# Performance work log

Hardware: AMD Instinct MI355X
Metric: run time of the kernel (lower is better)

The kernel has to match this reference:

```python
import jax, jax.numpy as jnp
import numpy as np

B, S, H = 2, 2048, 3072
NQ, NKV, HD = 24, 8, 128
ROT = 96  # floor(128 * 0.75)
BASE = 10000.0


def _rope(x, rotary_dim, base=BASE, start_index=0):
    # x: [b, s, h, rotary_dim]; keras_hub GPT-NeoX style half-rotation
    s = x.shape[1]
    inv_freq = 1.0 / (base ** (jnp.arange(0, rotary_dim, 2, dtype=jnp.float32) / rotary_dim))
    pos = jnp.arange(s, dtype=jnp.float32) + start_index
    freq = pos[:, None] * inv_freq[None, :]            # [s, rot/2]
    emb = jnp.concatenate([freq, freq], axis=-1)       # [s, rot]
    cos = jnp.cos(emb)[None, :, None, :]
    sin = jnp.sin(emb)[None, :, None, :]
    x1, x2 = jnp.split(x, 2, axis=-1)
    half_rot = jnp.concatenate([-x2, x1], axis=-1)
    return x * cos + half_rot * sin


def setup_inputs() -> dict:
    key = jax.random.key(0)
    k1, k2, k3, k4, k5 = jax.random.split(key, 5)
    hidden_states = jax.random.normal(k1, (B, S, H), dtype=jnp.float32)
    # causal mask [B, S, S]
    attention_mask = jnp.broadcast_to(jnp.tril(jnp.ones((S, S), dtype=bool)), (B, S, S))
    scale = 0.02
    Wq = jax.random.normal(k2, (H, NQ, HD), dtype=jnp.float32) * scale
    Wk = jax.random.normal(k3, (H, NKV, HD), dtype=jnp.float32) * scale
    Wv = jax.random.normal(k4, (H, NKV, HD), dtype=jnp.float32) * scale
    Wo = jax.random.normal(k5, (NQ, HD, H), dtype=jnp.float32) * scale
    return {"hidden_states": hidden_states, "attention_mask": attention_mask,
            "Wq": Wq, "Wk": Wk, "Wv": Wv, "Wo": Wo}


def reference(hidden_states, attention_mask, Wq, Wk, Wv, Wo):
    groups = NQ // NKV
    inv_norm = 1.0 / np.sqrt(HD)
    q = jnp.einsum('bqm,muh->bquh', hidden_states, Wq)   # [B,S,NQ,HD]
    k = jnp.einsum('bkm,mvh->bkvh', hidden_states, Wk)   # [B,S,NKV,HD]
    v = jnp.einsum('bkm,mvh->bkvh', hidden_states, Wv)
    # partial RoPE on first ROT dims
    q = jnp.concatenate([_rope(q[..., :ROT], ROT), q[..., ROT:]], axis=-1)
    k = jnp.concatenate([_rope(k[..., :ROT], ROT), k[..., ROT:]], axis=-1)
    # GQA: repeat kv heads (interleaved, matches ops.repeat axis=2)
    k = jnp.repeat(k, groups, axis=2)
    v = jnp.repeat(v, groups, axis=2)
    scores = jnp.einsum('bquh,bkuh->buqk', q, k) * inv_norm  # [B,NQ,S,S]
    scores = scores.astype(jnp.float32)
    scores = jnp.where(attention_mask[:, None, :, :], scores, -1e9)
    probs = jax.nn.softmax(scores, axis=-1).astype(hidden_states.dtype)
    attn = jnp.einsum('buqk,bkuh->bquh', probs, v)           # [B,S,NQ,HD]
    return jnp.einsum('bquh,uhm->bqm', attn, Wo)             # [B,S,H]
```

## Files before the change

### kernel.cpp

```cpp
#include <hip/hip_runtime.h>
#include <hip/hip_bf16.h>
#include <cstdint>

namespace {

constexpr int Bn = 2, Sn = 2048, Hn = 3072, NQn = 24, NKVn = 8, HDn = 128;
constexpr int LDQKV = NQn * HDn + 2 * NKVn * HDn;
constexpr int KCOLo = NQn * HDn;
constexpr int VCOLo = KCOLo + NKVn * HDn;

typedef __attribute__((ext_vector_type(8))) __bf16 bf16x8;
typedef __attribute__((ext_vector_type(4))) float f32x4;
typedef __attribute__((ext_vector_type(4))) unsigned short u16x4;

__device__ __forceinline__ unsigned short f2bf(float f) {
  union { float f; unsigned u; } v; v.f = f;
  return (unsigned short)((v.u + 0x7fffu + ((v.u >> 16) & 1u)) >> 16);
}
__device__ __forceinline__ float bf2f(unsigned short u) {
  union { unsigned u; float f; } v; v.u = ((unsigned)u) << 16;
  return v.f;
}
__device__ __forceinline__ void gload_lds16(const void* g, void* l) {
  __builtin_amdgcn_global_load_lds(
      (__attribute__((address_space(1))) void*)(uintptr_t)g,
      (__attribute__((address_space(3))) void*)(uintptr_t)l, 16, 0, 0);
}

__global__ void build_rope_tab(float* __restrict__ cosT, float* __restrict__ sinT) {
  int idx = blockIdx.x * 256 + threadIdx.x;
  if (idx >= Sn * 48) return;
  int s = idx / 48, i = idx % 48;
  float invf = exp2f(-(float)i * (13.287712379549449f / 48.f));
  float f = (float)s * invf;
  cosT[idx] = cosf(f);
  sinT[idx] = sinf(f);
}

__global__ void cvt_f32_bf16(const float* __restrict__ in, unsigned short* __restrict__ out, int n) {
  int i = (blockIdx.x * 256 + threadIdx.x) * 4;
  int stride = gridDim.x * 256 * 4;
  for (; i < n; i += stride) {
    float4 v = *(const float4*)&in[i];
    u16x4 o;
    o[0] = f2bf(v.x); o[1] = f2bf(v.y); o[2] = f2bf(v.z); o[3] = f2bf(v.w);
    *(u16x4*)&out[i] = o;
  }
}

__global__ void transpose_cvt(const float* __restrict__ in, unsigned short* __restrict__ out,
                              int K, int N) {
  __shared__ float tile[32][33];
  int bx = blockIdx.x * 32;
  int by = blockIdx.y * 32;
  int tx = threadIdx.x & 31, ty = threadIdx.x >> 5;
#pragma unroll
  for (int r = ty; r < 32; r += 8)
    tile[r][tx] = in[(size_t)(by + r) * N + bx + tx];
  __syncthreads();
#pragma unroll
  for (int r = ty; r < 32; r += 8)
    out[(size_t)(bx + r) * K + by + tx] = f2bf(tile[tx][r]);
}

__global__ void transpose_v(const unsigned short* __restrict__ QKV, unsigned short* __restrict__ VT) {
  __shared__ unsigned short tile[32][33];
  int s0 = blockIdx.x * 32;
  int b = blockIdx.y >> 5;
  int vc0 = (blockIdx.y & 31) * 32;
  int tx = threadIdx.x & 31, ty = threadIdx.x >> 5;
#pragma unroll
  for (int r = ty; r < 32; r += 8)
    tile[r][tx] = QKV[(size_t)(b * Sn + s0 + r) * LDQKV + VCOLo + vc0 + tx];
  __syncthreads();
#pragma unroll
  for (int r = ty; r < 32; r += 8)
    VT[(size_t)(b * (NKVn * HDn) + vc0 + r) * Sn + s0 + tx] = tile[tx][r];
}

template <int BF16OUT>
__launch_bounds__(512, 1)
__global__ void gemm256(const unsigned short* __restrict__ A, const unsigned short* __restrict__ Bm,
                        void* __restrict__ Cout, int M, int N, int K) {
  __shared__ unsigned short Al[2][256 * 64];
  __shared__ unsigned short Bl[2][256 * 64];
  const int t = threadIdx.x;
  const int lane = t & 63;
  const int w = t >> 6;
  const int wm = w >> 2, wn = w & 3;
  const int l15 = lane & 15, lq = lane >> 4;
  const int brow = blockIdx.y * 256, bcol = blockIdx.x * 256;
  const unsigned short* Ab = A + (size_t)brow * K;
  const unsigned short* Bb = Bm + (size_t)bcol * K;
  f32x4 acc[8][4] = {};
  const int nT = K >> 6;

  auto stage = [&](int kt, int buf) {
#pragma unroll
    for (int it = 0; it < 4; ++it) {
      int c = it * 512 + t;
      int row = c >> 3, pos = c & 7;
      int j = pos ^ (row & 7);
      gload_lds16(Ab + (size_t)row * K + kt * 64 + j * 8, (char*)&Al[buf][0] + c * 16);
    }
#pragma unroll
    for (int it = 0; it < 4; ++it) {
      int c = it * 512 + t;
      int row = c >> 3, pos = c & 7;
      int j = pos ^ (row & 7);
      gload_lds16(Bb + (size_t)row * K + kt * 64 + j * 8, (char*)&Bl[buf][0] + c * 16);
    }
  };

  stage(0, 0);
  stage(1, 1);
  for (int kt = 0; kt < nT; ++kt) {
    if (kt + 1 < nT) asm volatile("s_waitcnt vmcnt(8)" ::: "memory");
    else             asm volatile("s_waitcnt vmcnt(0)" ::: "memory");
    __builtin_amdgcn_s_barrier();
    __builtin_amdgcn_sched_barrier(0);
    const unsigned short* Abl = &Al[kt & 1][0];
    const unsigned short* Bbl = &Bl[kt & 1][0];
#pragma unroll
    for (int ks = 0; ks < 2; ++ks) {
      bf16x8 aF[8], bF[4];
      const int j = ks * 4 + lq;
#pragma unroll
      for (int m = 0; m < 8; ++m) {
        int row = wm * 128 + m * 16 + l15;
        aF[m] = *(const bf16x8*)&Abl[row * 64 + (j ^ (row & 7)) * 8];
      }
#pragma unroll
      for (int n = 0; n < 4; ++n) {
        int row = wn * 64 + n * 16 + l15;
        bF[n] = *(const bf16x8*)&Bbl[row * 64 + (j ^ (row & 7)) * 8];
      }
      __builtin_amdgcn_s_setprio(1);
#pragma unroll
      for (int m = 0; m < 8; ++m)
#pragma unroll
        for (int n = 0; n < 4; ++n)
          acc[m][n] = __builtin_amdgcn_mfma_f32_16x16x32_bf16(aF[m], bF[n], acc[m][n], 0, 0, 0);
      __builtin_amdgcn_s_setprio(0);
    }
    asm volatile("s_waitcnt lgkmcnt(0)" ::: "memory");
    __builtin_amdgcn_s_barrier();
    __builtin_amdgcn_sched_barrier(0);
    if (kt + 2 < nT) stage(kt + 2, kt & 1);
  }

  const int lr = lq * 4;
  if (BF16OUT) {
    unsigned short* C = (unsigned short*)Cout;
#pragma unroll
    for (int m = 0; m < 8; ++m) {
      int row = brow + wm * 128 + m * 16 + lr;
#pragma unroll
      for (int n = 0; n < 4; ++n) {
        int col = bcol + wn * 64 + n * 16 + l15;
#pragma unroll
        for (int i = 0; i < 4; ++i)
          C[(size_t)(row + i) * N + col] = f2bf(acc[m][n][i]);
      }
    }
  } else {
    float* C = (float*)Cout;
#pragma unroll
    for (int m = 0; m < 8; ++m) {
      int row = brow + wm * 128 + m * 16 + lr;
#pragma unroll
      for (int n = 0; n < 4; ++n) {
        int col = bcol + wn * 64 + n * 16 + l15;
#pragma unroll
        for (int i = 0; i < 4; ++i)
          C[(size_t)(row + i) * N + col] = acc[m][n][i];
      }
    }
  }
}

__global__ void rope_kernel(unsigned short* __restrict__ QKV, const float* __restrict__ cosT,
                            const float* __restrict__ sinT) {
  int rid = blockIdx.x;
  int s = rid & (Sn - 1);
  unsigned short* row = QKV + (size_t)rid * LDQKV;
  for (int p = threadIdx.x; p < 32 * 48; p += 256) {
    int h = p / 48, i = p % 48;
    int col = (h < NQn) ? h * HDn : KCOLo + (h - NQn) * HDn;
    float c = cosT[s * 48 + i], sn = sinT[s * 48 + i];
    float x1 = bf2f(row[col + i]), x2 = bf2f(row[col + i + 48]);
    row[col + i] = f2bf(x1 * c - x2 * sn);
    row[col + i + 48] = f2bf(x2 * c + x1 * sn);
  }
}

__launch_bounds__(256, 2)
__global__ void attn_kernel(const unsigned short* __restrict__ QKV,
                            const unsigned short* __restrict__ VT,
                            unsigned short* __restrict__ O) {
  __shared__ unsigned short Klds[2][64 * 128];
  __shared__ unsigned short Vlds[2][128 * 64];
  __shared__ unsigned short Plds[4][16 * 64];
  const int t = threadIdx.x, lane = t & 63, w = t >> 6;
  const int bq = gridDim.x - 1 - blockIdx.x;
  const int hid = blockIdx.y;
  const int b = hid / NQn, u = hid % NQn, kv = u / 3;
  const int l15 = lane & 15, lh = lane >> 4;

  bf16x8 qf[4];
  {
    int qrow = bq * 64 + w * 16 + l15;
    const unsigned short* qp = QKV + (size_t)(b * Sn + qrow) * LDQKV + u * HDn;
#pragma unroll
    for (int f = 0; f < 4; ++f) qf[f] = *(const bf16x8*)(qp + f * 32 + lh * 8);
  }
  float m_l = -1e30f, l_l = 0.f;
  f32x4 Oa[8] = {};
  const float cscale = 0.08838834764831845f * 1.4426950408889634f;

  const unsigned short* Kg = QKV + (size_t)(b * Sn) * LDQKV + KCOLo + kv * HDn;
  const unsigned short* Vg = VT + (size_t)(b * NKVn + kv) * HDn * Sn;

  auto stageK = [&](int kt, int buf) {
#pragma unroll
    for (int iter = 0; iter < 4; ++iter) {
      int c = iter * 256 + t;
      int krow = c >> 4, pch = c & 15;
      int hch = (pch & 8) | ((pch & 7) ^ (krow & 7));
      gload_lds16(Kg + (size_t)(kt * 64 + krow) * LDQKV + hch * 8,
                  (char*)&Klds[buf][0] + (iter * 256 + w * 64) * 16);
    }
  };
  auto stageV = [&](int kt, int buf) {
#pragma unroll
    for (int iter = 0; iter < 4; ++iter) {
      int c = iter * 256 + t;
      int hd = c >> 3, p = c & 7;
      int sch = p ^ (hd & 7);
      gload_lds16(Vg + (size_t)hd * Sn + kt * 64 + sch * 8,
                  (char*)&Vlds[buf][0] + (iter * 256 + w * 64) * 16);
    }
  };

  const int nt = bq + 1;
  stageK(0, 0);
  stageV(0, 0);
  __syncthreads();

  for (int kt = 0; kt < nt; ++kt) {
    const int cur = kt & 1;
    if (kt + 1 < nt) { stageK(kt + 1, cur ^ 1); stageV(kt + 1, cur ^ 1); }
    const unsigned short* Kb = &Klds[cur][0];
    const unsigned short* Vb = &Vlds[cur][0];
    f32x4 Sg[4] = {};
    __builtin_amdgcn_s_setprio(1);
#pragma unroll
    for (int g = 0; g < 4; ++g) {
      int kcol = g * 16 + l15;
#pragma unroll
      for (int s = 0; s < 4; ++s) {
        int h = s * 4 + lh;
        int p = (h & 8) | ((h & 7) ^ (kcol & 7));
        bf16x8 kf = *(const bf16x8*)&Kb[kcol * 128 + p * 8];
        Sg[g] = __builtin_amdgcn_mfma_f32_16x16x32_bf16(kf, qf[s], Sg[g], 0, 0, 0);
      }
    }
    __builtin_amdgcn_s_setprio(0);
    float P[4][4];
    const bool last = (kt == bq);
    const int qin = w * 16 + l15;
#pragma unroll
    for (int g = 0; g < 4; ++g)
#pragma unroll
      for (int i = 0; i < 4; ++i) {
        float sv = Sg[g][i] * cscale;
        if (last && (g * 16 + lh * 4 + i) > qin) sv = -1e30f;
        P[g][i] = sv;
      }
    float pmax = -1e30f;
#pragma unroll
    for (int g = 0; g < 4; ++g)
#pragma unroll
      for (int i = 0; i < 4; ++i) pmax = fmaxf(pmax, P[g][i]);
    pmax = fmaxf(pmax, __shfl_xor(pmax, 16, 64));
    pmax = fmaxf(pmax, __shfl_xor(pmax, 32, 64));
    float mn = fmaxf(m_l, pmax);
    float rs = exp2f(m_l - mn);
    m_l = mn;
    float ps = 0.f;
#pragma unroll
    for (int g = 0; g < 4; ++g)
#pragma unroll
      for (int i = 0; i < 4; ++i) {
        float e = exp2f(P[g][i] - mn);
        P[g][i] = e;
        ps += e;
      }
    ps += __shfl_xor(ps, 16, 64);
    ps += __shfl_xor(ps, 32, 64);
    l_l = l_l * rs + ps;
#pragma unroll
    for (int g = 0; g < 8; ++g)
#pragma unroll
      for (int i = 0; i < 4; ++i) Oa[g][i] *= rs;
    unsigned short* pl = Plds[w];
#pragma unroll
    for (int g = 0; g < 4; ++g) {
      int ch = g * 2 + (lh >> 1);
      int pos = ch ^ (l15 & 7);
      u16x4 pk;
#pragma unroll
      for (int i = 0; i < 4; ++i) pk[i] = f2bf(P[g][i]);
      *(u16x4*)&pl[l15 * 64 + pos * 8 + (lh & 1) * 4] = pk;
    }
    __builtin_amdgcn_s_setprio(1);
#pragma unroll
    for (int kk = 0; kk < 2; ++kk) {
      int ch = kk * 4 + lh;
      bf16x8 pf = *(const bf16x8*)&pl[l15 * 64 + ((ch ^ (l15 & 7)) & 7) * 8];
#pragma unroll
      for (int g = 0; g < 8; ++g) {
        int hd = g * 16 + l15;
        int vpos = (ch ^ (hd & 7)) & 7;
        bf16x8 vf = *(const bf16x8*)&Vb[hd * 64 + vpos * 8];
        Oa[g] = __builtin_amdgcn_mfma_f32_16x16x32_bf16(vf, pf, Oa[g], 0, 0, 0);
      }
    }
    __builtin_amdgcn_s_setprio(0);
    __syncthreads();
  }
  {
    unsigned short* sc = (unsigned short*)Klds + w * 2176;
    float inv = 1.0f / l_l;
#pragma unroll
    for (int g = 0; g < 8; ++g)
#pragma unroll
      for (int i = 0; i < 4; ++i)
        sc[l15 * 136 + g * 16 + lh * 4 + i] = f2bf(Oa[g][i] * inv);
    int q = lane >> 2, a = lane & 3;
    int row = bq * 64 + w * 16 + q;
    unsigned short* op = O + (size_t)(b * Sn + row) * (NQn * HDn) + u * HDn;
    const unsigned short* scr = sc + q * 136;
#pragma unroll
    for (int j = 0; j < 4; ++j) {
      bf16x8 v = *(const bf16x8*)&scr[a * 8 + j * 32];
      *(bf16x8*)&op[a * 8 + j * 32] = v;
    }
  }
}

}

extern "C" void kernel_launch(void* const* d_in, const int* in_sizes, int n_in,
                              void* d_out, int out_size, void* d_ws, size_t ws_size,
                              hipStream_t stream) {
  const float* hidden = (const float*)d_in[0];
  const float* Wq = (const float*)d_in[2];
  const float* Wk = (const float*)d_in[3];
  const float* Wv = (const float*)d_in[4];
  const float* Wo = (const float*)d_in[5];
  float* out = (float*)d_out;

  char* ws = (char*)d_ws;
  constexpr size_t szXb = (size_t)Bn * Sn * Hn * 2;
  constexpr size_t szWqkv = (size_t)LDQKV * Hn * 2;
  constexpr size_t szWo = (size_t)Hn * Hn * 2;
  constexpr size_t szVT = (size_t)Bn * NKVn * HDn * Sn * 2;
  constexpr size_t szQKV = (size_t)Bn * Sn * LDQKV * 2;
  constexpr size_t szTab = (size_t)Sn * 48 * 4;
  static_assert(szWo + szVT <= szWqkv, "Wob+VT must fit in Wqkv region");
  constexpr size_t szTotal = szXb + szWqkv + szQKV + 2 * szTab;
  if (ws_size < szTotal) return;

  unsigned short* Xb = (unsigned short*)(ws);
  unsigned short* Obuf = Xb;
  unsigned short* Wqkv = (unsigned short*)(ws + szXb);
  unsigned short* Wob = Wqkv;
  unsigned short* VT = (unsigned short*)(ws + szXb + szWo);
  unsigned short* QKV = (unsigned short*)(ws + szXb + szWqkv);
  float* cosT = (float*)(ws + szXb + szWqkv + szQKV);
  float* sinT = (float*)(ws + szXb + szWqkv + szQKV + szTab);

  build_rope_tab<<<(Sn * 48 + 255) / 256, 256, 0, stream>>>(cosT, sinT);
  cvt_f32_bf16<<<3072, 256, 0, stream>>>(hidden, Xb, Bn * Sn * Hn);
  transpose_cvt<<<dim3(96, 96), 256, 0, stream>>>(Wq, Wqkv, Hn, NQn * HDn);
  transpose_cvt<<<dim3(32, 96), 256, 0, stream>>>(Wk, Wqkv + (size_t)KCOLo * Hn, Hn, NKVn * HDn);
  transpose_cvt<<<dim3(32, 96), 256, 0, stream>>>(Wv, Wqkv + (size_t)VCOLo * Hn, Hn, NKVn * HDn);
  gemm256<1><<<dim3(LDQKV / 256, (Bn * Sn) / 256), 512, 0, stream>>>(Xb, Wqkv, QKV,
                                                                     Bn * Sn, LDQKV, Hn);
  transpose_cvt<<<dim3(96, 96), 256, 0, stream>>>(Wo, Wob, Hn, Hn);
  transpose_v<<<dim3(Sn / 32, Bn * NKVn * HDn / 32), 256, 0, stream>>>(QKV, VT);
  rope_kernel<<<Bn * Sn, 256, 0, stream>>>(QKV, cosT, sinT);
  attn_kernel<<<dim3(Sn / 64, Bn * NQn), 256, 0, stream>>>(QKV, VT, Obuf);
  gemm256<0><<<dim3(Hn / 256, (Bn * Sn) / 256), 512, 0, stream>>>(Obuf, Wob, out,
                                                                  Bn * Sn, Hn, Hn);
}
```

Baseline: 675.7 us.

## Double query tile per attention block to reuse K/V fragments across two subtiles

```diff
diff --git a/kernel.cpp b/kernel.cpp
--- a/kernel.cpp
+++ b/kernel.cpp
@@ -198,24 +198,27 @@
 __global__ void attn_kernel(const unsigned short* __restrict__ QKV,
                             const unsigned short* __restrict__ VT,
                             unsigned short* __restrict__ O) {
-  __shared__ unsigned short Klds[2][64 * 128];
-  __shared__ unsigned short Vlds[2][128 * 64];
-  __shared__ unsigned short Plds[4][16 * 64];
+  __shared__ __align__(16) char smem[81920];
+  unsigned short* Klds = (unsigned short*)smem;
+  unsigned short* Vlds = (unsigned short*)(smem + 32768);
+  unsigned short* Plds = (unsigned short*)(smem + 65536);
   const int t = threadIdx.x, lane = t & 63, w = t >> 6;
   const int bq = gridDim.x - 1 - blockIdx.x;
   const int hid = blockIdx.y;
   const int b = hid / NQn, u = hid % NQn, kv = u / 3;
   const int l15 = lane & 15, lh = lane >> 4;
-
-  bf16x8 qf[4];
-  {
-    int qrow = bq * 64 + w * 16 + l15;
+  const int q0 = bq * 128 + w * 32;
+
+  bf16x8 qf[2][4];
+#pragma unroll
+  for (int qs = 0; qs < 2; ++qs) {
+    int qrow = q0 + qs * 16 + l15;
     const unsigned short* qp = QKV + (size_t)(b * Sn + qrow) * LDQKV + u * HDn;
 #pragma unroll
-    for (int f = 0; f < 4; ++f) qf[f] = *(const bf16x8*)(qp + f * 32 + lh * 8);
-  }
-  float m_l = -1e30f, l_l = 0.f;
-  f32x4 Oa[8] = {};
+    for (int f = 0; f < 4; ++f) qf[qs][f] = *(const bf16x8*)(qp + f * 32 + lh * 8);
+  }
+  float m_l[2] = {-1e30f, -1e30f}, l_l[2] = {0.f, 0.f};
+  f32x4 Oa[2][8] = {};
   const float cscale = 0.08838834764831845f * 1.4426950408889634f;
 
   const unsigned short* Kg = QKV + (size_t)(b * Sn) * LDQKV + KCOLo + kv * HDn;
@@ -228,7 +231,7 @@
       int krow = c >> 4, pch = c & 15;
       int hch = (pch & 8) | ((pch & 7) ^ (krow & 7));
       gload_lds16(Kg + (size_t)(kt * 64 + krow) * LDQKV + hch * 8,
-                  (char*)&Klds[buf][0] + (iter * 256 + w * 64) * 16);
+                  (char*)Klds + buf * 16384 + (iter * 256 + w * 64) * 16);
     }
   };
   auto stageV = [&](int kt, int buf) {
@@ -238,11 +241,11 @@
       int hd = c >> 3, p = c & 7;
       int sch = p ^ (hd & 7);
       gload_lds16(Vg + (size_t)hd * Sn + kt * 64 + sch * 8,
-                  (char*)&Vlds[buf][0] + (iter * 256 + w * 64) * 16);
+                  (char*)Vlds + buf * 16384 + (iter * 256 + w * 64) * 16);
     }
   };
 
-  const int nt = bq + 1;
+  const int nt = 2 * bq + 2;
   stageK(0, 0);
   stageV(0, 0);
   __syncthreads();
@@ -250,101 +253,113 @@
   for (int kt = 0; kt < nt; ++kt) {
     const int cur = kt & 1;
     if (kt + 1 < nt) { stageK(kt + 1, cur ^ 1); stageV(kt + 1, cur ^ 1); }
-    const unsigned short* Kb = &Klds[cur][0];
-    const unsigned short* Vb = &Vlds[cur][0];
-    f32x4 Sg[4] = {};
-    __builtin_amdgcn_s_setprio(1);
-#pragma unroll
-    for (int g = 0; g < 4; ++g) {
-      int kcol = g * 16 + l15;
-#pragma unroll
-      for (int s = 0; s < 4; ++s) {
-        int h = s * 4 + lh;
-        int p = (h & 8) | ((h & 7) ^ (kcol & 7));
-        bf16x8 kf = *(const bf16x8*)&Kb[kcol * 128 + p * 8];
-        Sg[g] = __builtin_amdgcn_mfma_f32_16x16x32_bf16(kf, qf[s], Sg[g], 0, 0, 0);
-      }
-    }
-    __builtin_amdgcn_s_setprio(0);
-    float P[4][4];
-    const bool last = (kt == bq);
-    const int qin = w * 16 + l15;
-#pragma unroll
-    for (int g = 0; g < 4; ++g)
-#pragma unroll
-      for (int i = 0; i < 4; ++i) {
-        float sv = Sg[g][i] * cscale;
-        if (last && (g * 16 + lh * 4 + i) > qin) sv = -1e30f;
-        P[g][i] = sv;
-      }
-    float pmax = -1e30f;
-#pragma unroll
-    for (int g = 0; g < 4; ++g)
-#pragma unroll
-      for (int i = 0; i < 4; ++i) pmax = fmaxf(pmax, P[g][i]);
-    pmax = fmaxf(pmax, __shfl_xor(pmax, 16, 64));
-    pmax = fmaxf(pmax, __shfl_xor(pmax, 32, 64));
-    float mn = fmaxf(m_l, pmax);
-    float rs = exp2f(m_l - mn);
-    m_l = mn;
-    float ps = 0.f;
-#pragma unroll
-    for (int g = 0; g < 4; ++g)
-#pragma unroll
-      for (int i = 0; i < 4; ++i) {
-        float e = exp2f(P[g][i] - mn);
-        P[g][i] = e;
-        ps += e;
-      }
-    ps += __shfl_xor(ps, 16, 64);
-    ps += __shfl_xor(ps, 32, 64);
-    l_l = l_l * rs + ps;
-#pragma unroll
-    for (int g = 0; g < 8; ++g)
-#pragma unroll
-      for (int i = 0; i < 4; ++i) Oa[g][i] *= rs;
-    unsigned short* pl = Plds[w];
-#pragma unroll
-    for (int g = 0; g < 4; ++g) {
-      int ch = g * 2 + (lh >> 1);
-      int pos = ch ^ (l15 & 7);
-      u16x4 pk;
-#pragma unroll
-      for (int i = 0; i < 4; ++i) pk[i] = f2bf(P[g][i]);
-      *(u16x4*)&pl[l15 * 64 + pos * 8 + (lh & 1) * 4] = pk;
-    }
-    __builtin_amdgcn_s_setprio(1);
-#pragma unroll
-    for (int kk = 0; kk < 2; ++kk) {
-      int ch = kk * 4 + lh;
-      bf16x8 pf = *(const bf16x8*)&pl[l15 * 64 + ((ch ^ (l15 & 7)) & 7) * 8];
-#pragma unroll
-      for (int g = 0; g < 8; ++g) {
-        int hd = g * 16 + l15;
-        int vpos = (ch ^ (hd & 7)) & 7;
-        bf16x8 vf = *(const bf16x8*)&Vb[hd * 64 + vpos * 8];
-        Oa[g] = __builtin_amdgcn_mfma_f32_16x16x32_bf16(vf, pf, Oa[g], 0, 0, 0);
-      }
-    }
-    __builtin_amdgcn_s_setprio(0);
+    const unsigned short* Kb = Klds + cur * 8192;
+    const unsigned short* Vb = Vlds + cur * 8192;
+    if (kt * 64 <= q0 + 31) {
+      f32x4 Sg[2][4] = {};
+      __builtin_amdgcn_s_setprio(1);
+#pragma unroll
+      for (int g = 0; g < 4; ++g) {
+        int kcol = g * 16 + l15;
+#pragma unroll
+        for (int s = 0; s < 4; ++s) {
+          int h = s * 4 + lh;
+          int p = (h & 8) | ((h & 7) ^ (kcol & 7));
+          bf16x8 kf = *(const bf16x8*)&Kb[kcol * 128 + p * 8];
+          Sg[0][g] = __builtin_amdgcn_mfma_f32_16x16x32_bf16(kf, qf[0][s], Sg[0][g], 0, 0, 0);
+          Sg[1][g] = __builtin_amdgcn_mfma_f32_16x16x32_bf16(kf, qf[1][s], Sg[1][g], 0, 0, 0);
+        }
+      }
+      __builtin_amdgcn_s_setprio(0);
+      const bool maskT = kt * 64 + 63 > q0;
+#pragma unroll
+      for (int qs = 0; qs < 2; ++qs) {
+        float P[4][4];
+        const int qin = q0 + qs * 16 + l15;
+#pragma unroll
+        for (int g = 0; g < 4; ++g)
+#pragma unroll
+          for (int i = 0; i < 4; ++i) {
+            float sv = Sg[qs][g][i] * cscale;
+            if (maskT && (kt * 64 + g * 16 + lh * 4 + i) > qin) sv = -1e30f;
+            P[g][i] = sv;
+          }
+        float pmax = -1e30f;
+#pragma unroll
+        for (int g = 0; g < 4; ++g)
+#pragma unroll
+          for (int i = 0; i < 4; ++i) pmax = fmaxf(pmax, P[g][i]);
+        pmax = fmaxf(pmax, __shfl_xor(pmax, 16, 64));
+        pmax = fmaxf(pmax, __shfl_xor(pmax, 32, 64));
+        float mn = fmaxf(m_l[qs], pmax);
+        float rs = exp2f(m_l[qs] - mn);
+        m_l[qs] = mn;
+        float ps = 0.f;
+#pragma unroll
+        for (int g = 0; g < 4; ++g)
+#pragma unroll
+          for (int i = 0; i < 4; ++i) {
+            float e = exp2f(P[g][i] - mn);
+            P[g][i] = e;
+            ps += e;
+          }
+        ps += __shfl_xor(ps, 16, 64);
+        ps += __shfl_xor(ps, 32, 64);
+        l_l[qs] = l_l[qs] * rs + ps;
+#pragma unroll
+        for (int g = 0; g < 8; ++g)
+#pragma unroll
+          for (int i = 0; i < 4; ++i) Oa[qs][g][i] *= rs;
+        unsigned short* pl = Plds + w * 2048 + qs * 1024;
+#pragma unroll
+        for (int g = 0; g < 4; ++g) {
+          int ch = g * 2 + (lh >> 1);
+          int pos = ch ^ (l15 & 7);
+          u16x4 pk;
+#pragma unroll
+          for (int i = 0; i < 4; ++i) pk[i] = f2bf(P[g][i]);
+          *(u16x4*)&pl[l15 * 64 + pos * 8 + (lh & 1) * 4] = pk;
+        }
+      }
+      __builtin_amdgcn_s_setprio(1);
+#pragma unroll
+      for (int kk = 0; kk < 2; ++kk) {
+        int ch = kk * 4 + lh;
+        int ppos = ((ch ^ (l15 & 7)) & 7) * 8;
+        bf16x8 pf0 = *(const bf16x8*)&Plds[w * 2048 + l15 * 64 + ppos];
+        bf16x8 pf1 = *(const bf16x8*)&Plds[w * 2048 + 1024 + l15 * 64 + ppos];
+#pragma unroll
+        for (int g = 0; g < 8; ++g) {
+          int hd = g * 16 + l15;
+          int vpos = (ch ^ (hd & 7)) & 7;
+          bf16x8 vf = *(const bf16x8*)&Vb[hd * 64 + vpos * 8];
+          Oa[0][g] = __builtin_amdgcn_mfma_f32_16x16x32_bf16(vf, pf0, Oa[0][g], 0, 0, 0);
+          Oa[1][g] = __builtin_amdgcn_mfma_f32_16x16x32_bf16(vf, pf1, Oa[1][g], 0, 0, 0);
+        }
+      }
+      __builtin_amdgcn_s_setprio(0);
+    }
     __syncthreads();
   }
   {
-    unsigned short* sc = (unsigned short*)Klds + w * 2176;
-    float inv = 1.0f / l_l;
-#pragma unroll
-    for (int g = 0; g < 8; ++g)
-#pragma unroll
-      for (int i = 0; i < 4; ++i)
-        sc[l15 * 136 + g * 16 + lh * 4 + i] = f2bf(Oa[g][i] * inv);
-    int q = lane >> 2, a = lane & 3;
-    int row = bq * 64 + w * 16 + q;
+    unsigned short* sc = (unsigned short*)smem + w * 4352;
+#pragma unroll
+    for (int qs = 0; qs < 2; ++qs) {
+      float inv = 1.0f / l_l[qs];
+#pragma unroll
+      for (int g = 0; g < 8; ++g)
+#pragma unroll
+        for (int i = 0; i < 4; ++i)
+          sc[(qs * 16 + l15) * 136 + g * 16 + lh * 4 + i] = f2bf(Oa[qs][g][i] * inv);
+    }
+    int q = lane >> 1, a = lane & 1;
+    int row = bq * 128 + w * 32 + q;
     unsigned short* op = O + (size_t)(b * Sn + row) * (NQn * HDn) + u * HDn;
-    const unsigned short* scr = sc + q * 136;
-#pragma unroll
-    for (int j = 0; j < 4; ++j) {
-      bf16x8 v = *(const bf16x8*)&scr[a * 8 + j * 32];
-      *(bf16x8*)&op[a * 8 + j * 32] = v;
+    const unsigned short* scr = sc + q * 136 + a * 64;
+#pragma unroll
+    for (int j = 0; j < 8; ++j) {
+      bf16x8 v = *(const bf16x8*)&scr[j * 8];
+      *(bf16x8*)&op[a * 64 + j * 8] = v;
     }
   }
 }
@@ -391,7 +406,7 @@
   transpose_cvt<<<dim3(96, 96), 256, 0, stream>>>(Wo, Wob, Hn, Hn);
   transpose_v<<<dim3(Sn / 32, Bn * NKVn * HDn / 32), 256, 0, stream>>>(QKV, VT);
   rope_kernel<<<Bn * Sn, 256, 0, stream>>>(QKV, cosT, sinT);
-  attn_kernel<<<dim3(Sn / 64, Bn * NQn), 256, 0, stream>>>(QKV, VT, Obuf);
+  attn_kernel<<<dim3(Sn / 128, Bn * NQn), 256, 0, stream>>>(QKV, VT, Obuf);
   gemm256<0><<<dim3(Hn / 256, (Bn * Sn) / 256), 512, 0, stream>>>(Obuf, Wob, out,
                                                                   Bn * Sn, Hn, Hn);
 }
```

After: 675.4 us. No clear change (-0.1%).

## Double attention query tile to 128 rows with 8 waves, lazy softmax rescale

Applied to the files above, without the earlier changes.

```diff
diff --git a/kernel.cpp b/kernel.cpp
--- a/kernel.cpp
+++ b/kernel.cpp
@@ -194,22 +194,24 @@
   }
 }
 
-__launch_bounds__(256, 2)
+__launch_bounds__(512, 4)
 __global__ void attn_kernel(const unsigned short* __restrict__ QKV,
                             const unsigned short* __restrict__ VT,
                             unsigned short* __restrict__ O) {
-  __shared__ unsigned short Klds[2][64 * 128];
-  __shared__ unsigned short Vlds[2][128 * 64];
-  __shared__ unsigned short Plds[4][16 * 64];
+  __shared__ __align__(16) char smem[81920];
+  unsigned short* Klds = (unsigned short*)smem;
+  unsigned short* Vlds = (unsigned short*)(smem + 32768);
+  unsigned short* Plds = (unsigned short*)(smem + 65536);
   const int t = threadIdx.x, lane = t & 63, w = t >> 6;
   const int bq = gridDim.x - 1 - blockIdx.x;
   const int hid = blockIdx.y;
   const int b = hid / NQn, u = hid % NQn, kv = u / 3;
   const int l15 = lane & 15, lh = lane >> 4;
+  const int q0 = bq * 128 + w * 16;
 
   bf16x8 qf[4];
   {
-    int qrow = bq * 64 + w * 16 + l15;
+    int qrow = q0 + l15;
     const unsigned short* qp = QKV + (size_t)(b * Sn + qrow) * LDQKV + u * HDn;
 #pragma unroll
     for (int f = 0; f < 4; ++f) qf[f] = *(const bf16x8*)(qp + f * 32 + lh * 8);
@@ -223,26 +225,26 @@
 
   auto stageK = [&](int kt, int buf) {
 #pragma unroll
-    for (int iter = 0; iter < 4; ++iter) {
-      int c = iter * 256 + t;
+    for (int it = 0; it < 2; ++it) {
+      int c = it * 512 + t;
       int krow = c >> 4, pch = c & 15;
       int hch = (pch & 8) | ((pch & 7) ^ (krow & 7));
       gload_lds16(Kg + (size_t)(kt * 64 + krow) * LDQKV + hch * 8,
-                  (char*)&Klds[buf][0] + (iter * 256 + w * 64) * 16);
+                  (char*)Klds + buf * 16384 + c * 16);
     }
   };
   auto stageV = [&](int kt, int buf) {
 #pragma unroll
-    for (int iter = 0; iter < 4; ++iter) {
-      int c = iter * 256 + t;
+    for (int it = 0; it < 2; ++it) {
+      int c = it * 512 + t;
       int hd = c >> 3, p = c & 7;
       int sch = p ^ (hd & 7);
       gload_lds16(Vg + (size_t)hd * Sn + kt * 64 + sch * 8,
-                  (char*)&Vlds[buf][0] + (iter * 256 + w * 64) * 16);
+                  (char*)Vlds + buf * 16384 + c * 16);
     }
   };
 
-  const int nt = bq + 1;
+  const int nt = 2 * bq + 2;
   stageK(0, 0);
   stageV(0, 0);
   __syncthreads();
@@ -250,87 +252,92 @@
   for (int kt = 0; kt < nt; ++kt) {
     const int cur = kt & 1;
     if (kt + 1 < nt) { stageK(kt + 1, cur ^ 1); stageV(kt + 1, cur ^ 1); }
-    const unsigned short* Kb = &Klds[cur][0];
-    const unsigned short* Vb = &Vlds[cur][0];
-    f32x4 Sg[4] = {};
-    __builtin_amdgcn_s_setprio(1);
-#pragma unroll
-    for (int g = 0; g < 4; ++g) {
-      int kcol = g * 16 + l15;
-#pragma unroll
-      for (int s = 0; s < 4; ++s) {
-        int h = s * 4 + lh;
-        int p = (h & 8) | ((h & 7) ^ (kcol & 7));
-        bf16x8 kf = *(const bf16x8*)&Kb[kcol * 128 + p * 8];
-        Sg[g] = __builtin_amdgcn_mfma_f32_16x16x32_bf16(kf, qf[s], Sg[g], 0, 0, 0);
-      }
-    }
-    __builtin_amdgcn_s_setprio(0);
-    float P[4][4];
-    const bool last = (kt == bq);
-    const int qin = w * 16 + l15;
-#pragma unroll
-    for (int g = 0; g < 4; ++g)
-#pragma unroll
-      for (int i = 0; i < 4; ++i) {
-        float sv = Sg[g][i] * cscale;
-        if (last && (g * 16 + lh * 4 + i) > qin) sv = -1e30f;
-        P[g][i] = sv;
-      }
-    float pmax = -1e30f;
-#pragma unroll
-    for (int g = 0; g < 4; ++g)
-#pragma unroll
-      for (int i = 0; i < 4; ++i) pmax = fmaxf(pmax, P[g][i]);
-    pmax = fmaxf(pmax, __shfl_xor(pmax, 16, 64));
-    pmax = fmaxf(pmax, __shfl_xor(pmax, 32, 64));
-    float mn = fmaxf(m_l, pmax);
-    float rs = exp2f(m_l - mn);
-    m_l = mn;
-    float ps = 0.f;
-#pragma unroll
-    for (int g = 0; g < 4; ++g)
-#pragma unroll
-      for (int i = 0; i < 4; ++i) {
-        float e = exp2f(P[g][i] - mn);
-        P[g][i] = e;
-        ps += e;
-      }
-    ps += __shfl_xor(ps, 16, 64);
-    ps += __shfl_xor(ps, 32, 64);
-    l_l = l_l * rs + ps;
-#pragma unroll
-    for (int g = 0; g < 8; ++g)
-#pragma unroll
-      for (int i = 0; i < 4; ++i) Oa[g][i] *= rs;
-    unsigned short* pl = Plds[w];
-#pragma unroll
-    for (int g = 0; g < 4; ++g) {
-      int ch = g * 2 + (lh >> 1);
-      int pos = ch ^ (l15 & 7);
-      u16x4 pk;
-#pragma unroll
-      for (int i = 0; i < 4; ++i) pk[i] = f2bf(P[g][i]);
-      *(u16x4*)&pl[l15 * 64 + pos * 8 + (lh & 1) * 4] = pk;
-    }
-    __builtin_amdgcn_s_setprio(1);
-#pragma unroll
-    for (int kk = 0; kk < 2; ++kk) {
-      int ch = kk * 4 + lh;
-      bf16x8 pf = *(const bf16x8*)&pl[l15 * 64 + ((ch ^ (l15 & 7)) & 7) * 8];
-#pragma unroll
-      for (int g = 0; g < 8; ++g) {
-        int hd = g * 16 + l15;
-        int vpos = (ch ^ (hd & 7)) & 7;
-        bf16x8 vf = *(const bf16x8*)&Vb[hd * 64 + vpos * 8];
-        Oa[g] = __builtin_amdgcn_mfma_f32_16x16x32_bf16(vf, pf, Oa[g], 0, 0, 0);
-      }
-    }
-    __builtin_amdgcn_s_setprio(0);
+    const unsigned short* Kb = Klds + cur * 8192;
+    const unsigned short* Vb = Vlds + cur * 8192;
+    if (kt * 64 <= q0 + 15) {
+      f32x4 Sg[4] = {};
+      __builtin_amdgcn_s_setprio(1);
+#pragma unroll
+      for (int g = 0; g < 4; ++g) {
+        int kcol = g * 16 + l15;
+#pragma unroll
+        for (int s = 0; s < 4; ++s) {
+          int h = s * 4 + lh;
+          int p = (h & 8) | ((h & 7) ^ (kcol & 7));
+          bf16x8 kf = *(const bf16x8*)&Kb[kcol * 128 + p * 8];
+          Sg[g] = __builtin_amdgcn_mfma_f32_16x16x32_bf16(kf, qf[s], Sg[g], 0, 0, 0);
+        }
+      }
+      __builtin_amdgcn_s_setprio(0);
+      float P[4][4];
+      const bool maskT = kt * 64 + 63 > q0;
+      const int qin = q0 + l15;
+#pragma unroll
+      for (int g = 0; g < 4; ++g)
+#pragma unroll
+        for (int i = 0; i < 4; ++i) {
+          float sv = Sg[g][i] * cscale;
+          if (maskT && (kt * 64 + g * 16 + lh * 4 + i) > qin) sv = -1e30f;
+          P[g][i] = sv;
+        }
+      float pmax = -1e30f;
+#pragma unroll
+      for (int g = 0; g < 4; ++g)
+#pragma unroll
+        for (int i = 0; i < 4; ++i) pmax = fmaxf(pmax, P[g][i]);
+      pmax = fmaxf(pmax, __shfl_xor(pmax, 16, 64));
+      pmax = fmaxf(pmax, __shfl_xor(pmax, 32, 64));
+      if (__any(pmax > m_l + 8.0f)) {
+        float mn = fmaxf(m_l, pmax);
+        float rs = exp2f(m_l - mn);
+        m_l = mn;
+        l_l *= rs;
+#pragma unroll
+        for (int g = 0; g < 8; ++g)
+#pragma unroll
+          for (int i = 0; i < 4; ++i) Oa[g][i] *= rs;
+      }
+      float ps = 0.f;
+#pragma unroll
+      for (int g = 0; g < 4; ++g)
+#pragma unroll
+        for (int i = 0; i < 4; ++i) {
+          float e = exp2f(P[g][i] - m_l);
+          P[g][i] = e;
+          ps += e;
+        }
+      ps += __shfl_xor(ps, 16, 64);
+      ps += __shfl_xor(ps, 32, 64);
+      l_l += ps;
+      unsigned short* pl = Plds + w * 1024;
+#pragma unroll
+      for (int g = 0; g < 4; ++g) {
+        int ch = g * 2 + (lh >> 1);
+        int pos = ch ^ (l15 & 7);
+        union { unsigned u2[2]; u16x4 v4; } pk;
+        asm("v_cvt_pk_bf16_f32 %0, %1, %2" : "=v"(pk.u2[0]) : "v"(P[g][0]), "v"(P[g][1]));
+        asm("v_cvt_pk_bf16_f32 %0, %1, %2" : "=v"(pk.u2[1]) : "v"(P[g][2]), "v"(P[g][3]));
+        *(u16x4*)&pl[l15 * 64 + pos * 8 + (lh & 1) * 4] = pk.v4;
+      }
+      __builtin_amdgcn_s_setprio(1);
+#pragma unroll
+      for (int kk = 0; kk < 2; ++kk) {
+        int ch = kk * 4 + lh;
+        bf16x8 pf = *(const bf16x8*)&pl[l15 * 64 + ((ch ^ (l15 & 7)) & 7) * 8];
+#pragma unroll
+        for (int g = 0; g < 8; ++g) {
+          int hd = g * 16 + l15;
+          int vpos = (ch ^ (hd & 7)) & 7;
+          bf16x8 vf = *(const bf16x8*)&Vb[hd * 64 + vpos * 8];
+          Oa[g] = __builtin_amdgcn_mfma_f32_16x16x32_bf16(vf, pf, Oa[g], 0, 0, 0);
+        }
+      }
+      __builtin_amdgcn_s_setprio(0);
+    }
     __syncthreads();
   }
   {
-    unsigned short* sc = (unsigned short*)Klds + w * 2176;
+    unsigned short* sc = (unsigned short*)smem + w * 2176;
     float inv = 1.0f / l_l;
 #pragma unroll
     for (int g = 0; g < 8; ++g)
@@ -338,7 +345,7 @@
       for (int i = 0; i < 4; ++i)
         sc[l15 * 136 + g * 16 + lh * 4 + i] = f2bf(Oa[g][i] * inv);
     int q = lane >> 2, a = lane & 3;
-    int row = bq * 64 + w * 16 + q;
+    int row = q0 + q;
     unsigned short* op = O + (size_t)(b * Sn + row) * (NQn * HDn) + u * HDn;
     const unsigned short* scr = sc + q * 136;
 #pragma unroll
@@ -391,7 +398,7 @@
   transpose_cvt<<<dim3(96, 96), 256, 0, stream>>>(Wo, Wob, Hn, Hn);
   transpose_v<<<dim3(Sn / 32, Bn * NKVn * HDn / 32), 256, 0, stream>>>(QKV, VT);
   rope_kernel<<<Bn * Sn, 256, 0, stream>>>(QKV, cosT, sinT);
-  attn_kernel<<<dim3(Sn / 64, Bn * NQn), 256, 0, stream>>>(QKV, VT, Obuf);
+  attn_kernel<<<dim3(Sn / 128, Bn * NQn), 512, 0, stream>>>(QKV, VT, Obuf);
   gemm256<0><<<dim3(Hn / 256, (Bn * Sn) / 256), 512, 0, stream>>>(Obuf, Wob, out,
                                                                   Bn * Sn, Hn, Hn);
 }
```

Result: faster. 642.0 us (-5.0%).
